# Kernel tuning notes

Hardware: AMD Instinct MI355X
Metric: run time of the kernel (lower is better)

The kernel has to match this reference:

```python
import jax, jax.numpy as jnp
import numpy as np

M, K, N = 8192, 4096, 12288


def setup_inputs() -> dict:
    key = jax.random.key(0)
    k1, k2, k3, k4 = jax.random.split(key, 4)
    input_tensor = jax.random.normal(k1, (1, M, K), dtype=jnp.float32)
    # int8 quantized weight [N, K] and per-output-channel scale [N, 1]
    weight = jax.random.randint(k2, (N, K), -127, 128, dtype=jnp.int32).astype(jnp.int8)
    weight_scale = (jax.random.uniform(k3, (N, 1), dtype=jnp.float32) * 0.01 + 1e-4)
    bias = jax.random.normal(k4, (N,), dtype=jnp.float32) * 0.1
    return {"input_tensor": input_tensor, "weight": weight,
            "weight_scale": weight_scale, "bias": bias}


def reference(input_tensor, weight, weight_scale, bias):
    x = input_tensor[0]  # squeeze(0) -> [M, K]
    # dynamic per-token symmetric int8 quantization: scale = absmax/127
    a_scale = jnp.max(jnp.abs(x), axis=-1, keepdims=True) / 127.0  # [M, 1]
    q = jnp.clip(jnp.round(x / a_scale), -128.0, 127.0)  # int8 values held in f32
    # int8 GEMM accumulated (emulated in f32), then dequant with per-token x per-channel scales
    acc = jnp.einsum('mk,nk->mn', q, weight.astype(jnp.float32))  # [M, N]
    out = acc * a_scale * weight_scale[:, 0][None, :] + bias[None, :]
    return out[None].astype(input_tensor.dtype)  # unsqueeze(0) -> [1, M, N]
```

## Files before the change

kernel.cpp:

```cpp
#include <hip/hip_runtime.h>
#include <cstdint>

#define M_DIM 8192
#define K_DIM 4096
#define N_DIM 12288
#define KT 32

using i32x4 = __attribute__((ext_vector_type(4))) int;

__device__ inline void gload_lds16(const void* g, void* l) {
    __builtin_amdgcn_global_load_lds(
        (const __attribute__((address_space(1))) void*)g,
        (__attribute__((address_space(3))) void*)l,
        16, 0, 0);
}

__device__ inline int pack4(int4 v) {
    return (v.x & 255) | ((v.y & 255) << 8) | ((v.z & 255) << 16) | (v.w << 24);
}

__global__ __launch_bounds__(256) void quant_pack(const float* __restrict__ x,
                                                  const int* __restrict__ w32,
                                                  int8_t* __restrict__ qa,
                                                  float* __restrict__ ascale,
                                                  int8_t* __restrict__ wb) {
    const int t = threadIdx.x;
    if (blockIdx.x < M_DIM) {
        const int row = blockIdx.x;
        const float4* xr = (const float4*)(x + (size_t)row * K_DIM);
        float4 v[4];
        float amax = 0.0f;
#pragma unroll
        for (int c = 0; c < 4; ++c) {
            v[c] = xr[t + 256 * c];
            amax = fmaxf(amax, fmaxf(fmaxf(fabsf(v[c].x), fabsf(v[c].y)),
                                     fmaxf(fabsf(v[c].z), fabsf(v[c].w))));
        }
#pragma unroll
        for (int off = 32; off > 0; off >>= 1)
            amax = fmaxf(amax, __shfl_xor(amax, off));
        __shared__ float smax[4];
        if ((t & 63) == 0) smax[t >> 6] = amax;
        __syncthreads();
        amax = fmaxf(fmaxf(smax[0], smax[1]), fmaxf(smax[2], smax[3]));
        const float sc = amax * (1.0f / 127.0f);
        const float inv = (amax > 0.0f) ? (127.0f / amax) : 0.0f;
        if (t == 0) ascale[row] = sc;

        int* q32 = (int*)(qa + (size_t)row * K_DIM);
#pragma unroll
        for (int c = 0; c < 4; ++c) {
            int q0 = (int)rintf(v[c].x * inv);
            int q1 = (int)rintf(v[c].y * inv);
            int q2 = (int)rintf(v[c].z * inv);
            int q3 = (int)rintf(v[c].w * inv);
            q0 = min(127, max(-128, q0));
            q1 = min(127, max(-128, q1));
            q2 = min(127, max(-128, q2));
            q3 = min(127, max(-128, q3));
            q32[t + 256 * c] = (q0 & 255) | ((q1 & 255) << 8) | ((q2 & 255) << 16) | (q3 << 24);
        }
    } else {
        const int pb = blockIdx.x - M_DIM;
        const size_t total = (size_t)N_DIM * K_DIM / 16;
        const size_t stride = (size_t)2048 * 256;
        for (size_t i = (size_t)pb * 256 + t; i < total; i += stride) {
            const uint32_t c = (uint32_t)i;
            const int lr = c & 15;
            const int lk = (c >> 4) & 3;
            const uint32_t q = c >> 6;
            const int ks = q & 1;
            const int nf = (q >> 1) & 3;
            const uint32_t r = q >> 3;
            const int j = r & 31;
            const uint32_t s2 = r >> 5;
            const int n = (int)(s2 >> 2) * 256 + (int)(s2 & 3) * 64 + nf * 16 + lr;
            const int k0 = j * 128 + (ks * 4 + lk) * 16;
            const int4* src = (const int4*)(w32 + (size_t)n * K_DIM + k0);
            const int4 v0 = src[0], v1 = src[1], v2 = src[2], v3 = src[3];
            i32x4 o;
            o[0] = pack4(v0); o[1] = pack4(v1); o[2] = pack4(v2); o[3] = pack4(v3);
            ((i32x4*)wb)[i] = o;
        }
    }
}

__global__ __launch_bounds__(512, 2) void gemm_i8(const int8_t* __restrict__ qa,
                                                  const int8_t* __restrict__ wb,
                                                  const float* __restrict__ ascale,
                                                  const float* __restrict__ wscale,
                                                  const float* __restrict__ bias,
                                                  float* __restrict__ out) {
    __shared__ int8_t lds[2][32768];

    const int t = threadIdx.x;
    const int lane = t & 63;
    const int wave = t >> 6;
    const int wm = wave >> 2;
    const int wn = wave & 3;
    const int lrow = lane & 15;
    const int lk = lane >> 4;
    const int sw7 = lrow & 7;

    const int flat = blockIdx.x;
    const int sw = (flat & 7) * 192 + (flat >> 3);
    const int bm = sw / 48;
    const int bn = sw % 48;

    const int srow = t >> 3;
    const int g = (t & 7) ^ (srow & 7);

#define STAGE_A(sb, jt)                                                        \
    {                                                                          \
        _Pragma("unroll") for (int c = 0; c < 4; ++c)                          \
            gload_lds16(qa + (size_t)(bm * 256 + srow + 64 * c) * K_DIM +      \
                            (size_t)g * 16 + (size_t)(jt) * 128,               \
                        &lds[sb][c * 8192 + t * 16]);                          \
    }
#define READ_A(dst, cs, mh)                                                    \
    {                                                                          \
        _Pragma("unroll") for (int mf = 0; mf < 4; ++mf)                       \
            _Pragma("unroll") for (int ks = 0; ks < 2; ++ks)                   \
                dst[mf][ks] = *(const i32x4*)&lds[cs][(wm * 128 + (mh)*64 +    \
                                                      mf * 16 + lrow) * 128 + \
                                                     ((((ks << 2) | lk) ^ sw7) << 4)]; \
    }
    const int8_t* wbase = wb + (size_t)(bn * 4 + wn) * 262144 + (size_t)lane * 16;
#define LOAD_BLO(jt)                                                           \
    {                                                                          \
        _Pragma("unroll") for (int nf = 0; nf < 2; ++nf)                       \
            _Pragma("unroll") for (int ks = 0; ks < 2; ++ks)                   \
                bLo[nf][ks] = *(const i32x4*)(wbase + (size_t)(jt)*8192 +      \
                                              (nf * 2 + ks) * 1024);           \
    }
#define LOAD_BHI(jt)                                                           \
    {                                                                          \
        _Pragma("unroll") for (int nf = 0; nf < 2; ++nf)                       \
            _Pragma("unroll") for (int ks = 0; ks < 2; ++ks)                   \
                bHi[nf][ks] = *(const i32x4*)(wbase + (size_t)(jt)*8192 +      \
                                              ((nf + 2) * 2 + ks) * 1024);     \
    }
#define MM8(AH, mb, BH, nb)                                                    \
    {                                                                          \
        __builtin_amdgcn_s_setprio(1);                                         \
        _Pragma("unroll") for (int ks = 0; ks < 2; ++ks)                       \
            _Pragma("unroll") for (int mf = 0; mf < 4; ++mf)                   \
                _Pragma("unroll") for (int nf = 0; nf < 2; ++nf)               \
                    acc[(mb) + mf][(nb) + nf] =                                \
                        __builtin_amdgcn_mfma_i32_16x16x64_i8(                 \
                            AH[mf][ks], BH[nf][ks],                            \
                            acc[(mb) + mf][(nb) + nf], 0, 0, 0);               \
        __builtin_amdgcn_s_setprio(0);                                         \
    }
#define SB0 __builtin_amdgcn_sched_barrier(0);
#define BAR __builtin_amdgcn_s_barrier();
#define WAIT_LGKM(n) asm volatile("s_waitcnt lgkmcnt(" #n ")" ::: "memory");
#define WAIT_VM(n) asm volatile("s_waitcnt vmcnt(" #n ")" ::: "memory");

    i32x4 acc[8][4] = {};
    i32x4 a0[4][2], a1[4][2], bLo[2][2], bHi[2][2];

    STAGE_A(0, 0);
    LOAD_BLO(0);
    LOAD_BHI(0);
    SB0;

    for (int j = 0; j < KT; ++j) {
        const int cs = j & 1;
        const int ns = cs ^ 1;

        WAIT_VM(4);
        SB0;
        BAR;
        SB0;
        if (j + 1 < KT) STAGE_A(ns, j + 1);
        READ_A(a0, cs, 0);
        READ_A(a1, cs, 1);
        SB0;
        WAIT_LGKM(8);
        SB0;
        MM8(a0, 0, bLo, 0);
        WAIT_LGKM(0);
        SB0;
        MM8(a1, 4, bLo, 0);
        if (j + 1 < KT) {
            LOAD_BLO(j + 1);
            SB0;
            WAIT_VM(8);
        } else {
            WAIT_VM(0);
        }
        SB0;
        MM8(a1, 4, bHi, 2);
        MM8(a0, 0, bHi, 2);
        if (j + 1 < KT) LOAD_BHI(j + 1);
        SB0;
    }

    const int r0 = bm * 256 + wm * 128;
    const int c0 = bn * 256 + wn * 64;
    float asc[8][4];
#pragma unroll
    for (int m = 0; m < 8; ++m)
#pragma unroll
        for (int jj = 0; jj < 4; ++jj)
            asc[m][jj] = ascale[r0 + m * 16 + lk * 4 + jj];
#pragma unroll
    for (int n = 0; n < 4; ++n) {
        const int col = c0 + n * 16 + lrow;
        const float wsc = wscale[col];
        const float bb = bias[col];
#pragma unroll
        for (int m = 0; m < 8; ++m) {
#pragma unroll
            for (int jj = 0; jj < 4; ++jj) {
                const int row = r0 + m * 16 + lk * 4 + jj;
                out[(size_t)row * N_DIM + col] = (float)acc[m][n][jj] * asc[m][jj] * wsc + bb;
            }
        }
    }
}

extern "C" void kernel_launch(void* const* d_in, const int* in_sizes, int n_in,
                              void* d_out, int out_size, void* d_ws, size_t ws_size,
                              hipStream_t stream) {
    const float* x = (const float*)d_in[0];
    const int* w32 = (const int*)d_in[1];
    const float* wscale = (const float*)d_in[2];
    const float* bias = (const float*)d_in[3];
    float* out = (float*)d_out;

    int8_t* qa = (int8_t*)d_ws;
    float* ascale = (float*)((char*)d_ws + (size_t)M_DIM * K_DIM);
    int8_t* wb = (int8_t*)((char*)d_ws + (size_t)M_DIM * K_DIM +
                           (size_t)M_DIM * sizeof(float));

    quant_pack<<<M_DIM + 2048, 256, 0, stream>>>(x, w32, qa, ascale, wb);
    gemm_i8<<<1536, 512, 0, stream>>>(qa, wb, ascale, wscale, bias, out);
}
```

Measured before the change: 552.9 us.

## Give each wave private LDS A tiles and drop block-level barriers

The int8 GEMM main loop now has each wave stage its own 128-row A slice into a private double-buffered LDS region, halving the K-step to 64. This removes the per-iteration block barrier. B fragments are loaded per half-tile into two register sets that alternate, and the loop is unrolled by two. The cost is that the four waves sharing rows now each fetch those A rows separately, so global/L2 traffic for A roughly quadruples. LDS usage also doubles to 128KB, which likely prevents two blocks from fitting per CU.

```diff
diff --git a/kernel.cpp b/kernel.cpp
--- a/kernel.cpp
+++ b/kernel.cpp
@@ -4,7 +4,7 @@
 #define M_DIM 8192
 #define K_DIM 4096
 #define N_DIM 12288
-#define KT 32
+#define KT 64
 
 using i32x4 = __attribute__((ext_vector_type(4))) int;
 
@@ -91,7 +91,7 @@
                                                   const float* __restrict__ wscale,
                                                   const float* __restrict__ bias,
                                                   float* __restrict__ out) {
-    __shared__ int8_t lds[2][32768];
+    __shared__ int8_t lds[8][2][8192];
 
     const int t = threadIdx.x;
     const int lane = t & 63;
@@ -100,101 +100,71 @@
     const int wn = wave & 3;
     const int lrow = lane & 15;
     const int lk = lane >> 4;
-    const int sw7 = lrow & 7;
+    const int rslot = (lk ^ ((lrow >> 1) & 3)) << 4;
 
     const int flat = blockIdx.x;
     const int sw = (flat & 7) * 192 + (flat >> 3);
     const int bm = sw / 48;
     const int bn = sw % 48;
 
-    const int srow = t >> 3;
-    const int g = (t & 7) ^ (srow & 7);
+    const int g = (lane & 3) ^ ((lane >> 3) & 3);
+    const size_t abase = (size_t)(bm * 256 + wm * 128 + (lane >> 2)) * K_DIM +
+                         (size_t)g * 16;
 
 #define STAGE_A(sb, jt)                                                        \
     {                                                                          \
-        _Pragma("unroll") for (int c = 0; c < 4; ++c)                          \
-            gload_lds16(qa + (size_t)(bm * 256 + srow + 64 * c) * K_DIM +      \
-                            (size_t)g * 16 + (size_t)(jt) * 128,               \
-                        &lds[sb][c * 8192 + t * 16]);                          \
-    }
-#define READ_A(dst, cs, mh)                                                    \
+        _Pragma("unroll") for (int c = 0; c < 8; ++c)                          \
+            gload_lds16(qa + abase + (size_t)(c * 16) * K_DIM +                \
+                            (size_t)(jt) * 64,                                 \
+                        &lds[wave][sb][c * 1024 + lane * 16]);                 \
+    }
+    const int8_t* wbase = wb + (size_t)(bn * 4 + wn) * 262144 + (size_t)lane * 16;
+#define LOAD_B(dst, jt)                                                        \
     {                                                                          \
-        _Pragma("unroll") for (int mf = 0; mf < 4; ++mf)                       \
-            _Pragma("unroll") for (int ks = 0; ks < 2; ++ks)                   \
-                dst[mf][ks] = *(const i32x4*)&lds[cs][(wm * 128 + (mh)*64 +    \
-                                                      mf * 16 + lrow) * 128 + \
-                                                     ((((ks << 2) | lk) ^ sw7) << 4)]; \
-    }
-    const int8_t* wbase = wb + (size_t)(bn * 4 + wn) * 262144 + (size_t)lane * 16;
-#define LOAD_BLO(jt)                                                           \
-    {                                                                          \
-        _Pragma("unroll") for (int nf = 0; nf < 2; ++nf)                       \
-            _Pragma("unroll") for (int ks = 0; ks < 2; ++ks)                   \
-                bLo[nf][ks] = *(const i32x4*)(wbase + (size_t)(jt)*8192 +      \
-                                              (nf * 2 + ks) * 1024);           \
-    }
-#define LOAD_BHI(jt)                                                           \
-    {                                                                          \
-        _Pragma("unroll") for (int nf = 0; nf < 2; ++nf)                       \
-            _Pragma("unroll") for (int ks = 0; ks < 2; ++ks)                   \
-                bHi[nf][ks] = *(const i32x4*)(wbase + (size_t)(jt)*8192 +      \
-                                              ((nf + 2) * 2 + ks) * 1024);     \
-    }
-#define MM8(AH, mb, BH, nb)                                                    \
-    {                                                                          \
-        __builtin_amdgcn_s_setprio(1);                                         \
-        _Pragma("unroll") for (int ks = 0; ks < 2; ++ks)                       \
-            _Pragma("unroll") for (int mf = 0; mf < 4; ++mf)                   \
-                _Pragma("unroll") for (int nf = 0; nf < 2; ++nf)               \
-                    acc[(mb) + mf][(nb) + nf] =                                \
-                        __builtin_amdgcn_mfma_i32_16x16x64_i8(                 \
-                            AH[mf][ks], BH[nf][ks],                            \
-                            acc[(mb) + mf][(nb) + nf], 0, 0, 0);               \
-        __builtin_amdgcn_s_setprio(0);                                         \
+        _Pragma("unroll") for (int nf = 0; nf < 4; ++nf)                       \
+            dst[nf] = *(const i32x4*)(wbase + (size_t)((jt) >> 1) * 8192 +     \
+                                      (nf * 2 + ((jt)&1)) * 1024);             \
     }
 #define SB0 __builtin_amdgcn_sched_barrier(0);
-#define BAR __builtin_amdgcn_s_barrier();
 #define WAIT_LGKM(n) asm volatile("s_waitcnt lgkmcnt(" #n ")" ::: "memory");
 #define WAIT_VM(n) asm volatile("s_waitcnt vmcnt(" #n ")" ::: "memory");
 
     i32x4 acc[8][4] = {};
-    i32x4 a0[4][2], a1[4][2], bLo[2][2], bHi[2][2];
+    i32x4 a[8], b0[4], b1[4];
+
+#define TILE(J, BC, BN)                                                        \
+    {                                                                          \
+        WAIT_VM(4);                                                            \
+        SB0;                                                                   \
+        _Pragma("unroll") for (int mf = 0; mf < 8; ++mf)                       \
+            a[mf] = *(const i32x4*)&lds[wave][(J)&1][(mf * 16 + lrow) * 64 +   \
+                                                    rslot];                    \
+        if ((J) + 1 < KT) {                                                    \
+            STAGE_A(((J) + 1) & 1, (J) + 1);                                   \
+            LOAD_B(BN, (J) + 1);                                               \
+            WAIT_VM(12);                                                       \
+        } else {                                                               \
+            WAIT_VM(0);                                                        \
+        }                                                                      \
+        SB0;                                                                   \
+        WAIT_LGKM(0);                                                          \
+        SB0;                                                                   \
+        __builtin_amdgcn_s_setprio(1);                                         \
+        _Pragma("unroll") for (int mf = 0; mf < 8; ++mf)                       \
+            _Pragma("unroll") for (int nf = 0; nf < 4; ++nf)                   \
+                acc[mf][nf] = __builtin_amdgcn_mfma_i32_16x16x64_i8(           \
+                    a[mf], BC[nf], acc[mf][nf], 0, 0, 0);                      \
+        __builtin_amdgcn_s_setprio(0);                                         \
+        SB0;                                                                   \
+    }
 
     STAGE_A(0, 0);
-    LOAD_BLO(0);
-    LOAD_BHI(0);
+    LOAD_B(b0, 0);
     SB0;
 
-    for (int j = 0; j < KT; ++j) {
-        const int cs = j & 1;
-        const int ns = cs ^ 1;
-
-        WAIT_VM(4);
-        SB0;
-        BAR;
-        SB0;
-        if (j + 1 < KT) STAGE_A(ns, j + 1);
-        READ_A(a0, cs, 0);
-        READ_A(a1, cs, 1);
-        SB0;
-        WAIT_LGKM(8);
-        SB0;
-        MM8(a0, 0, bLo, 0);
-        WAIT_LGKM(0);
-        SB0;
-        MM8(a1, 4, bLo, 0);
-        if (j + 1 < KT) {
-            LOAD_BLO(j + 1);
-            SB0;
-            WAIT_VM(8);
-        } else {
-            WAIT_VM(0);
-        }
-        SB0;
-        MM8(a1, 4, bHi, 2);
-        MM8(a0, 0, bHi, 2);
-        if (j + 1 < KT) LOAD_BHI(j + 1);
-        SB0;
+    for (int j = 0; j < KT; j += 2) {
+        TILE(j, b0, b1);
+        TILE(j + 1, b1, b0);
     }
 
     const int r0 = bm * 256 + wm * 128;
```

Result: slower. 662.8 us (+19.9%).
